# Kernel tuning notes

Measured on AMD Instinct MI355X. Metric: run time of the kernel, lower is better.

Reference implementation:

```python
import jax, jax.numpy as jnp
import numpy as np

N, E, IN, H, T = 100000, 1600000, 10, 64, 10


def setup_inputs() -> dict:
    key = jax.random.key(0)
    ks = jax.random.split(key, 24)
    w = lambda k, shape, s=0.05: jax.random.normal(k, shape, jnp.float32) * s
    return {
        "x": w(ks[0], (N, IN), 1.0),
        "edge_attr": w(ks[1], (E, T), 1.0),
        "gcn1_w": w(ks[2], (IN, H)), "gcn1_b": jnp.zeros((H,), jnp.float32),
        "e_w1": w(ks[3], (3 * T, H)), "e_b1": jnp.zeros((H,), jnp.float32),
        "e_w2": w(ks[4], (H, H)), "e_b2": jnp.zeros((H,), jnp.float32),
        "gcn2_w": w(ks[5], (2 * H, H)), "gcn2_b": jnp.zeros((H,), jnp.float32),
        "gcn3_w": w(ks[6], (H, IN)), "gcn3_b": jnp.zeros((IN,), jnp.float32),
        "l1_w": w(ks[7], (2 * IN, IN)), "l1_b": jnp.zeros((IN,), jnp.float32),
        "l2_w": w(ks[8], (IN, 128)), "l2_b": jnp.zeros((128,), jnp.float32),
        "l3_w": w(ks[9], (128, 32)), "l3_b": jnp.zeros((32,), jnp.float32),
        "l4_w": w(ks[10], (32, 2)), "l4_b": jnp.zeros((2,), jnp.float32),
        "edge_index": jax.random.randint(ks[11], (2, E), 0, N),
    }


def reference(x, edge_attr, gcn1_w, gcn1_b, e_w1, e_b1, e_w2, e_b2,
              gcn2_w, gcn2_b, gcn3_w, gcn3_b, l1_w, l1_b, l2_w, l2_b,
              l3_w, l3_b, l4_w, l4_b, edge_index):
    src, dst = edge_index[0], edge_index[1]  # j -> i (message flows src->dst)
    # GCN symmetric norm with self loops: deg counted on target, +1 self loop
    deg = 1.0 + jax.ops.segment_sum(jnp.ones((E,), jnp.float32), dst, num_segments=N)
    dis = deg ** -0.5  # [N]
    edge_norm = (dis[src] * dis[dst])[:, None]  # [E,1]

    def gcn(h, w, b):
        hw = h @ w  # [N,out]
        agg = jax.ops.segment_sum(hw[src] * edge_norm, dst, num_segments=N)
        agg = agg + hw * (dis * dis)[:, None]  # self-loop term, norm = 1/deg
        return agg + b

    out1 = jax.nn.relu(gcn(x, gcn1_w, gcn1_b))
    # EdgeConv: gather x_i (dst), x_j (src), concat edge_attr, MLP, scatter-max
    m = jnp.concatenate([x[dst], x[src], edge_attr], axis=1)  # [E, 3T]
    m = jax.nn.relu(m @ e_w1 + e_b1) @ e_w2 + e_b2  # [E, H]
    agg = jax.ops.segment_max(m, dst, num_segments=N)
    agg = jnp.where(jnp.isfinite(agg), agg, 0.0)  # isolated nodes -> 0
    oute = jax.nn.relu(agg)

    out2 = jax.nn.relu(gcn(jnp.concatenate([out1, oute], axis=1), gcn2_w, gcn2_b))
    out3 = jax.nn.relu(gcn(out2, gcn3_w, gcn3_b))
    h = jnp.concatenate([x, out3], axis=1)  # [N, 2*IN]
    h = jax.nn.softplus(h @ l1_w + l1_b)
    h = jax.nn.softplus(h @ l2_w + l2_b)
    h = jax.nn.softplus(h @ l3_w + l3_b)
    h = h @ l4_w + l4_b  # [N, 2]
    return (h[:, 0], h[:, 1])
```

## Files before the change

kernel.cpp:

```cpp
#include <hip/hip_runtime.h>
#include <hip/hip_bf16.h>

typedef unsigned int u32;
typedef unsigned short u16;
typedef _Float16 f16;
typedef _Float16 f16x8 __attribute__((ext_vector_type(8)));
typedef float f32x4 __attribute__((ext_vector_type(4)));
typedef u32 u32x4 __attribute__((ext_vector_type(4)));

#define DEV static __device__ __forceinline__

#define O_G1   0
#define O_G1b  640
#define O_W1   704
#define O_B1   2624
#define O_W2   2688
#define O_B2   6784
#define O_G2   6848
#define O_G2b  15040
#define O_G3   15104
#define O_G3b  15744
#define O_L1   15754
#define O_L1b  15954
#define O_L2t  15964
#define O_L2b  17244
#define O_L3   17372
#define O_L3b  21468
#define O_L4t  21500
#define O_L4b  21564
#define O_WF1  21568
#define O_WF2  22592
#define WTOT   24640

#define ECNB   32

DEV float bfu(u16 h){ return __uint_as_float(((u32)h) << 16); }
DEV float bflo(u32 u){ return __uint_as_float(u << 16); }
DEV float bfhi(u32 u){ return __uint_as_float(u & 0xffff0000u); }
DEV u16 f2bf(float x){
  __hip_bfloat16 b = __float2bfloat16(x);
  return *(u16*)&b;
}
DEV float rdf(const void* p, int idx, int isf32){
  return isf32 ? ((const float*)p)[idx] : bfu(((const u16*)p)[idx]);
}
DEV void load10_bf(const u32* __restrict__ p, float* f){
  u32 a0=p[0],a1=p[1],a2=p[2],a3=p[3],a4=p[4];
  f[0]=bflo(a0); f[1]=bfhi(a0);
  f[2]=bflo(a1); f[3]=bfhi(a1);
  f[4]=bflo(a2); f[5]=bfhi(a2);
  f[6]=bflo(a3); f[7]=bfhi(a3);
  f[8]=bflo(a4); f[9]=bfhi(a4);
}
DEV void load10_any(const void* base, size_t row, int isf32, float* f){
  if (isf32){
    const float* p = (const float*)base + row*10;
    #pragma unroll
    for (int k=0;k<10;k++) f[k] = p[k];
  } else {
    load10_bf((const u32*)base + row*5, f);
  }
}
DEV f16 load1_f16(const void* base, long idx, int isf32){
  return isf32 ? (f16)((const float*)base)[idx] : (f16)bfu(((const u16*)base)[idx]);
}
DEV float softplusf(float x){ return fmaxf(x,0.f) + log1pf(__expf(-fabsf(x))); }

DEV int permk(int k){
  if (k < 8)  return k;
  if (k < 16) return 10 + (k-8);
  if (k < 24) return 20 + (k-16);
  if (k == 24) return 8;
  if (k == 25) return 9;
  if (k == 26) return 18;
  if (k == 27) return 19;
  if (k == 28) return 28;
  if (k == 29) return 29;
  return -1;
}
DEV u32 packh2(float a, float b){
  union { f16 h[2]; u32 u; } t;
  t.h[0] = (f16)a; t.h[1] = (f16)b;
  return t.u;
}

__global__ __launch_bounds__(256) void k_detect(
    const u32* p0, const u32* p1, const u32* p2, const u32* p3,
    const u32* p4, const u32* p5, const u32* p6, const u32* p7,
    const u32* p8, const u32* p9, const u32* p10,const u32* p11,
    const u32* p12,const u32* p13,const u32* p14,const u32* p15,
    const u32* p16,const u32* p17,const u32* p18,const u32* p19,
    int* __restrict__ flags, int N_, int E_)
{
  int a = blockIdx.x;
  const u32* p;
  int elems;
  switch (a){
    case 0:  p=p0;  elems=N_*10; break;
    case 1:  p=p1;  elems=E_*10; break;
    case 2:  p=p2;  elems=640;  break;
    case 3:  p=p3;  elems=64;   break;
    case 4:  p=p4;  elems=1920; break;
    case 5:  p=p5;  elems=64;   break;
    case 6:  p=p6;  elems=4096; break;
    case 7:  p=p7;  elems=64;   break;
    case 8:  p=p8;  elems=8192; break;
    case 9:  p=p9;  elems=64;   break;
    case 10: p=p10; elems=640;  break;
    case 11: p=p11; elems=10;   break;
    case 12: p=p12; elems=200;  break;
    case 13: p=p13; elems=10;   break;
    case 14: p=p14; elems=1280; break;
    case 15: p=p15; elems=128;  break;
    case 16: p=p16; elems=4096; break;
    case 17: p=p17; elems=32;   break;
    case 18: p=p18; elems=64;   break;
    default: p=p19; elems=2;    break;
  }
  int nw = elems/2; if (nw > 512) nw = 512; if (nw < 1) nw = 1;
  int localA = 0, localZ = 0;
  for (int i=threadIdx.x; i<nw; i+=256){
    u32 w = p[i];
    u32 ex = (w >> 7) & 0xffu;
    if (ex >= 0x90u) localA++;
    if ((w & 0xffffu) == 0u) localZ++;
  }
  int packed = (localA << 16) | localZ;
  __shared__ int red[4];
  #pragma unroll
  for (int off=32; off; off>>=1) packed += __shfl_down(packed, off);
  if ((threadIdx.x & 63) == 0) red[threadIdx.x>>6] = packed;
  __syncthreads();
  if (threadIdx.x == 0){
    int s = red[0]+red[1]+red[2]+red[3];
    int sA = s >> 16, sZ = s & 0xffff;
    flags[a] = (sA * 16 >= nw || sZ * 4 >= nw * 3) ? 1 : 0;
  }
}

__global__ __launch_bounds__(256) void k_prep(
    const void* g1w, const void* g1b, const void* ew1, const void* eb1,
    const void* ew2, const void* eb2, const void* g2w, const void* g2b,
    const void* g3w, const void* g3b, const void* l1w, const void* l1b,
    const void* l2w, const void* l2b, const void* l3w, const void* l3b,
    const void* l4w, const void* l4b,
    const int* __restrict__ flags, float* __restrict__ W)
{
  int t = threadIdx.x;
  int f2=flags[2],f3=flags[3],f4=flags[4],f5=flags[5],f6=flags[6],f7=flags[7];
  int f8=flags[8],f9=flags[9],f10=flags[10],f11=flags[11],f12=flags[12],f13=flags[13];
  int f14=flags[14],f15=flags[15],f16=flags[16],f17=flags[17],f18=flags[18],f19=flags[19];
  for (int i=t;i<640;i+=256)  W[O_G1+i]  = rdf(g1w,i,f2);
  for (int i=t;i<64;i+=256)   W[O_G1b+i] = rdf(g1b,i,f3);
  for (int i=t;i<1920;i+=256) W[O_W1+i]  = rdf(ew1,i,f4);
  for (int i=t;i<64;i+=256)   W[O_B1+i]  = rdf(eb1,i,f5);
  for (int i=t;i<4096;i+=256) W[O_W2+i]  = rdf(ew2,i,f6);
  for (int i=t;i<64;i+=256)   W[O_B2+i]  = rdf(eb2,i,f7);
  for (int i=t;i<8192;i+=256) W[O_G2+i]  = rdf(g2w,i,f8);
  for (int i=t;i<64;i+=256)   W[O_G2b+i] = rdf(g2b,i,f9);
  for (int i=t;i<640;i+=256)  W[O_G3+i]  = rdf(g3w,i,f10);
  for (int i=t;i<10;i+=256)   W[O_G3b+i] = rdf(g3b,i,f11);
  for (int i=t;i<200;i+=256)  W[O_L1+i]  = rdf(l1w,i,f12);
  for (int i=t;i<10;i+=256)   W[O_L1b+i] = rdf(l1b,i,f13);
  for (int i=t;i<1280;i+=256){ int o=i/10,k=i-o*10; W[O_L2t+i]=rdf(l2w,k*128+o,f14); }
  for (int i=t;i<128;i+=256)  W[O_L2b+i] = rdf(l2b,i,f15);
  for (int i=t;i<4096;i+=256) W[O_L3+i]  = rdf(l3w,i,f16);
  for (int i=t;i<32;i+=256)   W[O_L3b+i] = rdf(l3b,i,f17);
  for (int i=t;i<64;i+=256){ int c=i>>5,j=i&31; W[O_L4t+i]=rdf(l4w,j*2+c,f18); }
  for (int i=t;i<2;i+=256)    W[O_L4b+i] = rdf(l4b,i,f19);
  u32* Wu = (u32*)W;
  for (int i=t;i<1024;i+=256){
    int l=i&63, q=(i>>6)&3, c=i>>8;
    int k0=(l>>4)*8+2*q, col=c*16+(l&15);
    int r0=permk(k0), r1=permk(k0+1);
    float v0 = (r0<0)?0.f:rdf(ew1,r0*64+col,f4);
    float v1 = (r1<0)?0.f:rdf(ew1,r1*64+col,f4);
    Wu[O_WF1+i] = packh2(v0,v1);
  }
  for (int i=t;i<2048;i+=256){
    int l=i&63, q=(i>>6)&3, h2=(i>>8)&1, c=i>>9;
    int k0=32*h2+(l>>4)*8+2*q, col=c*16+(l&15);
    Wu[O_WF2+i] = packh2(rdf(ew2,k0*64+col,f6), rdf(ew2,(k0+1)*64+col,f6));
  }
}

__global__ __launch_bounds__(256) void k_init(int* __restrict__ cnt, int N_)
{
  int i = blockIdx.x*256 + threadIdx.x;
  if (i < N_) cnt[i] = 0;
}

__global__ __launch_bounds__(256) void k_count(const int* __restrict__ ei, int* __restrict__ cnt, int E_)
{
  int e = blockIdx.x*256 + threadIdx.x;
  if (e >= E_) return;
  atomicAdd(&cnt[ei[E_+e]], 1);
}

__global__ __launch_bounds__(1024) void k_bsum(const int* __restrict__ cnt, int* __restrict__ bsum, int N_)
{
  int i = blockIdx.x*1024 + threadIdx.x;
  int v = (i < N_) ? cnt[i] : 0;
  #pragma unroll
  for (int off=32; off; off>>=1) v += __shfl_down(v, off);
  __shared__ int ws_[16];
  if ((threadIdx.x & 63) == 0) ws_[threadIdx.x>>6] = v;
  __syncthreads();
  if (threadIdx.x == 0){
    int s = 0;
    #pragma unroll
    for (int j=0;j<16;j++) s += ws_[j];
    bsum[blockIdx.x] = s;
  }
}

__global__ __launch_bounds__(128) void k_scan_small(const int* __restrict__ bsum, int* __restrict__ boff, int NB)
{
  int t = threadIdx.x;
  int v = (t < NB) ? bsum[t] : 0;
  int lane = t & 63, w = t >> 6;
  int x = v;
  #pragma unroll
  for (int off=1; off<64; off<<=1){ int y=__shfl_up(x,off); if (lane>=off) x+=y; }
  __shared__ int t2[2];
  if (lane==63) t2[w]=x;
  __syncthreads();
  if (w==1) x += t2[0];
  boff[t] = x - v;
}

__global__ __launch_bounds__(1024) void k_scan_final(
    int* __restrict__ cnt, const int* __restrict__ boff,
    int* __restrict__ rp, float* __restrict__ dis, int N_, int E_)
{
  int i = blockIdx.x*1024 + threadIdx.x;
  int v = (i < N_) ? cnt[i] : 0;
  int lane = threadIdx.x & 63, w = threadIdx.x >> 6;
  int x = v;
  #pragma unroll
  for (int off=1; off<64; off<<=1){ int y=__shfl_up(x,off); if (lane>=off) x+=y; }
  __shared__ int wp[16];
  if (lane==63) wp[w]=x;
  __syncthreads();
  if (threadIdx.x==0){
    int run=0;
    #pragma unroll
    for (int j=0;j<16;j++){ int t=wp[j]; wp[j]=run; run+=t; }
  }
  __syncthreads();
  int incl = x + wp[w] + boff[blockIdx.x];
  if (i < N_){
    rp[i]  = incl - v;
    dis[i] = rsqrtf(1.f + (float)v);
    cnt[i] = 0;
  }
  if (i == 0) rp[N_] = E_;
}

__global__ __launch_bounds__(256) void k_fill(
    const int* __restrict__ ei, const int* __restrict__ rp, int* __restrict__ cnt,
    int* __restrict__ csrc, int* __restrict__ cedge, int* __restrict__ cdst, int E_)
{
  int e = blockIdx.x*256 + threadIdx.x;
  if (e >= E_) return;
  int s = ei[e], d = ei[E_+e];
  int pos = rp[d] + atomicAdd(&cnt[d], 1);
  csrc[pos]  = s;
  cedge[pos] = e;
  cdst[pos]  = d;
}

#define EC_EMIT \
  if (run >= 0){ int bb = run*64 + x; \
    atomicMax(&nodemax[bb],    __float_as_int(e0)); \
    atomicMax(&nodemax[bb+16], __float_as_int(e1)); \
    atomicMax(&nodemax[bb+32], __float_as_int(e2)); \
    atomicMax(&nodemax[bb+48], __float_as_int(e3)); }
#define EC_STEP(DD, RR) { \
  float t0=fmaxf(mcv[0][RR],0.f), t1=fmaxf(mcv[1][RR],0.f), \
        t2=fmaxf(mcv[2][RR],0.f), t3=fmaxf(mcv[3][RR],0.f); \
  if (DD == run){ e0=fmaxf(e0,t0); e1=fmaxf(e1,t1); e2=fmaxf(e2,t2); e3=fmaxf(e3,t3); } \
  else { EC_EMIT; run = DD; e0=t0; e1=t1; e2=t2; e3=t3; } }

__global__ __launch_bounds__(256) void k_edgeconv(
    const void* __restrict__ xv, const void* __restrict__ eav,
    const int* __restrict__ rp, const int* __restrict__ csrc,
    const int* __restrict__ cedge, const int* __restrict__ cdst,
    const float* __restrict__ W, const int* __restrict__ flags,
    float* __restrict__ oute, int N_, int E_)
{
  __shared__ int nodemax[ECNB*64];
  __shared__ u32 hbuf[4][16*36];
  int tid = threadIdx.x;
  int l = tid & 63, wv = tid >> 6;
  int x = l & 15, g = l >> 4;
  int n0 = blockIdx.x * ECNB;
  if (n0 >= N_) return;
  int nend = n0 + ECNB; if (nend > N_) nend = N_;
  #pragma unroll
  for (int i=0;i<ECNB/4;i++) nodemax[i*256 + tid] = 0;
  int fx = flags[0], fea = flags[1];
  const u32* Wu = (const u32*)W;
  union FU { u32 u[4]; f16x8 v; };
  FU w1u[4];
  #pragma unroll
  for (int c=0;c<4;c++){
    #pragma unroll
    for (int q=0;q<4;q++) w1u[c].u[q] = Wu[O_WF1 + (c*4+q)*64 + l];
  }
  FU w2u[4][2];
  #pragma unroll
  for (int c=0;c<4;c++){
    #pragma unroll
    for (int h=0;h<2;h++){
      #pragma unroll
      for (int q=0;q<4;q++) w2u[c][h].u[q] = Wu[O_WF2 + ((c*2+h)*4+q)*64 + l];
    }
  }
  float b1v[4], b2v[4];
  #pragma unroll
  for (int c=0;c<4;c++){ b1v[c] = (W+O_B1)[c*16 + x]; b2v[c] = (W+O_B2)[c*16 + x]; }
  int pbase = rp[n0], pend = rp[nend];
  int ntiles = (pend - pbase + 15) >> 4;
  u32* hb = hbuf[wv];
  __syncthreads();

  for (int t = wv; t < ntiles; t += 4){
    int p0 = pbase + t*16;
    int pe = p0 + 4*g;
    int d0 = (pe   < pend) ? cdst[pe]   - n0 : -1;
    int d1 = (pe+1 < pend) ? cdst[pe+1] - n0 : -1;
    int d2 = (pe+2 < pend) ? cdst[pe+2] - n0 : -1;
    int d3 = (pe+3 < pend) ? cdst[pe+3] - n0 : -1;
    int eA = p0 + x; if (eA > E_-1) eA = E_-1;
    union HU { f16 h[8]; u32 u[4]; f16x8 v; } af;
    if (g < 3){
      long row; const void* base; int isf;
      if (g==0){ row = cdst[eA];  base = xv;  isf = fx; }
      else if (g==1){ row = csrc[eA]; base = xv;  isf = fx; }
      else { row = cedge[eA]; base = eav; isf = fea; }
      if (isf){
        const float* p = (const float*)base + row*10;
        #pragma unroll
        for (int j=0;j<8;j++) af.h[j] = (f16)p[j];
      } else {
        const u32* p = (const u32*)((const u16*)base + row*10);
        #pragma unroll
        for (int j=0;j<4;j++){ u32 w = p[j]; af.h[2*j] = (f16)bflo(w); af.h[2*j+1] = (f16)bfhi(w); }
      }
    } else {
      int di = cdst[eA], si = csrc[eA], ee = cedge[eA];
      af.h[0] = load1_f16(xv, (long)di*10+8, fx);
      af.h[1] = load1_f16(xv, (long)di*10+9, fx);
      af.h[2] = load1_f16(xv, (long)si*10+8, fx);
      af.h[3] = load1_f16(xv, (long)si*10+9, fx);
      af.h[4] = load1_f16(eav,(long)ee*10+8, fea);
      af.h[5] = load1_f16(eav,(long)ee*10+9, fea);
      af.h[6] = (f16)0.f; af.h[7] = (f16)0.f;
    }
    f32x4 z = {0.f,0.f,0.f,0.f};
    f32x4 hc[4];
    #pragma unroll
    for (int c=0;c<4;c++)
      hc[c] = __builtin_amdgcn_mfma_f32_16x16x32_f16(af.v, w1u[c].v, z, 0, 0, 0);
    #pragma unroll
    for (int r=0;r<4;r++){
      u32 pk0,pk1,pk2,pk3;
      {
        float hv = fmaxf(hc[0][r] + b1v[0], 0.f);
        union { f16 h; u16 u; } cv; cv.h=(f16)hv; u32 mine=cv.u;
        u32 other=(u32)__shfl_xor((int)mine,1,64);
        pk0 = (x&1) ? (other|(mine<<16)) : (mine|(other<<16));
      }{
        float hv = fmaxf(hc[1][r] + b1v[1], 0.f);
        union { f16 h; u16 u; } cv; cv.h=(f16)hv; u32 mine=cv.u;
        u32 other=(u32)__shfl_xor((int)mine,1,64);
        pk1 = (x&1) ? (other|(mine<<16)) : (mine|(other<<16));
      }{
        float hv = fmaxf(hc[2][r] + b1v[2], 0.f);
        union { f16 h; u16 u; } cv; cv.h=(f16)hv; u32 mine=cv.u;
        u32 other=(u32)__shfl_xor((int)mine,1,64);
        pk2 = (x&1) ? (other|(mine<<16)) : (mine|(other<<16));
      }{
        float hv = fmaxf(hc[3][r] + b1v[3], 0.f);
        union { f16 h; u16 u; } cv; cv.h=(f16)hv; u32 mine=cv.u;
        u32 other=(u32)__shfl_xor((int)mine,1,64);
        pk3 = (x&1) ? (other|(mine<<16)) : (mine|(other<<16));
      }
      int edge = 4*g + r;
      int par = (x&1) ? 16 : 0;
      hb[edge*36 + par + (x>>1)]     = (x&1) ? pk2 : pk0;
      hb[edge*36 + 8 + par + (x>>1)] = (x&1) ? pk3 : pk1;
    }
    asm volatile("s_waitcnt lgkmcnt(0)" ::: "memory");
    HU a2f[2];
    #pragma unroll
    for (int h=0;h<2;h++){
      const u32x4* p = (const u32x4*)&hb[x*36 + g*4 + 16*h];
      u32x4 tv = *p;
      a2f[h].u[0]=tv[0]; a2f[h].u[1]=tv[1]; a2f[h].u[2]=tv[2]; a2f[h].u[3]=tv[3];
    }
    f32x4 mcv[4];
    #pragma unroll
    for (int c=0;c<4;c++){
      f32x4 bi = {b2v[c],b2v[c],b2v[c],b2v[c]};
      f32x4 acc = __builtin_amdgcn_mfma_f32_16x16x32_f16(a2f[0].v, w2u[c][0].v, bi, 0, 0, 0);
      mcv[c]    = __builtin_amdgcn_mfma_f32_16x16x32_f16(a2f[1].v, w2u[c][1].v, acc, 0, 0, 0);
    }
    int run = -2; float e0=0.f,e1=0.f,e2=0.f,e3=0.f;
    EC_STEP(d0,0) EC_STEP(d1,1) EC_STEP(d2,2) EC_STEP(d3,3)
    EC_EMIT;
  }
  __syncthreads();
  int tot = (nend - n0) * 64;
  for (int i = tid; i < tot; i += 256)
    oute[(size_t)n0*64 + i] = __int_as_float(nodemax[i]);
}

__global__ __launch_bounds__(256) void k_aggx(
    const void* __restrict__ xv, const int* __restrict__ rp,
    const int* __restrict__ csrc, const float* __restrict__ dis,
    const int* __restrict__ flags, float* __restrict__ sx, int N_)
{
  int i = blockIdx.x*256 + threadIdx.x;
  if (i >= N_) return;
  int fx = flags[0];
  float di = dis[i], d2 = di*di;
  float acc[10], ac2[10], tA[10], tB[10];
  load10_any(xv, (size_t)i, fx, tA);
  #pragma unroll
  for (int f=0;f<10;f++){ acc[f] = tA[f]*d2; ac2[f] = 0.f; }
  int b = rp[i], en = rp[i+1];
  int p = b;
  for (; p+1 < en; p += 2){
    int sA = csrc[p], sB = csrc[p+1];
    float nmA = dis[sA]*di, nmB = dis[sB]*di;
    load10_any(xv, (size_t)sA, fx, tA);
    load10_any(xv, (size_t)sB, fx, tB);
    #pragma unroll
    for (int f=0;f<10;f++){
      acc[f] = fmaf(tA[f], nmA, acc[f]);
      ac2[f] = fmaf(tB[f], nmB, ac2[f]);
    }
  }
  if (p < en){
    int sA = csrc[p]; float nmA = dis[sA]*di;
    load10_any(xv, (size_t)sA, fx, tA);
    #pragma unroll
    for (int f=0;f<10;f++) acc[f] = fmaf(tA[f], nmA, acc[f]);
  }
  float* o = sx + (size_t)i*10;
  #pragma unroll
  for (int f=0;f<10;f++) o[f] = acc[f] + ac2[f];
}

__global__ __launch_bounds__(256) void k_hw2(
    const float* __restrict__ sx, const float* __restrict__ oute,
    const float* __restrict__ W, u16* __restrict__ hw2o, int N_)
{
  int i = blockIdx.x*256 + threadIdx.x;
  if (i >= N_) return;
  float sv[10];
  const float* srow = sx + (size_t)i*10;
  #pragma unroll
  for (int f=0;f<10;f++) sv[f] = srow[f];
  const float* __restrict__ G1  = W + O_G1;
  const float* __restrict__ G1b = W + O_G1b;
  const float* __restrict__ G2  = W + O_G2;
  float hw[64];
  #pragma unroll
  for (int f=0;f<64;f++) hw[f] = 0.f;
  #pragma unroll 1
  for (int k=0;k<64;k++){
    float o1 = G1b[k];
    #pragma unroll
    for (int j=0;j<10;j++) o1 = fmaf(sv[j], G1[j*64+k], o1);
    o1 = fmaxf(o1, 0.f);
    const float* __restrict__ wt = G2 + k*64;
    #pragma unroll
    for (int f=0;f<64;f++) hw[f] = fmaf(o1, wt[f], hw[f]);
  }
  const float* orow = oute + (size_t)i*64;
  #pragma unroll 1
  for (int k=0;k<64;k++){
    float ov = orow[k];
    const float* __restrict__ wb = G2 + (64+k)*64;
    #pragma unroll
    for (int f=0;f<64;f++) hw[f] = fmaf(ov, wb[f], hw[f]);
  }
  u16* out = hw2o + (size_t)i*64;
  #pragma unroll
  for (int f=0;f<64;f++) out[f] = f2bf(hw[f]);
}

__global__ __launch_bounds__(256) void k_agg64(
    const u16* __restrict__ hw2, const int* __restrict__ rp,
    const int* __restrict__ csrc, const float* __restrict__ dis,
    const float* __restrict__ W, float* __restrict__ out2, int N_)
{
  int i = (blockIdx.x*256 + threadIdx.x) >> 6;
  int lane = threadIdx.x & 63;
  if (i >= N_) return;
  int e4 = lane >> 4, c4 = lane & 15;
  float di = dis[i];
  int b = rp[i], en = rp[i+1];
  const uint2* __restrict__ h2 = (const uint2*)hw2;
  float a0=0.f,a1=0.f,a2=0.f,a3=0.f;
  float b0=0.f,b1=0.f,b2=0.f,b3=0.f;
  int p = b + e4;
  int sA = (p   < en) ? csrc[p]   : 0;
  int sB = (p+4 < en) ? csrc[p+4] : 0;
  for (; p + 4 < en; p += 8){
    int sAn = (p+8  < en) ? csrc[p+8]  : 0;
    int sBn = (p+12 < en) ? csrc[p+12] : 0;
    float nmA = dis[sA]*di, nmB = dis[sB]*di;
    uint2 wA = h2[(size_t)sA*16 + c4];
    uint2 wB = h2[(size_t)sB*16 + c4];
    a0 = fmaf(bflo(wA.x), nmA, a0); a1 = fmaf(bfhi(wA.x), nmA, a1);
    a2 = fmaf(bflo(wA.y), nmA, a2); a3 = fmaf(bfhi(wA.y), nmA, a3);
    b0 = fmaf(bflo(wB.x), nmB, b0); b1 = fmaf(bfhi(wB.x), nmB, b1);
    b2 = fmaf(bflo(wB.y), nmB, b2); b3 = fmaf(bfhi(wB.y), nmB, b3);
    sA = sAn; sB = sBn;
  }
  if (p < en){
    float nmA = dis[sA]*di;
    uint2 wA = h2[(size_t)sA*16 + c4];
    a0 = fmaf(bflo(wA.x), nmA, a0); a1 = fmaf(bfhi(wA.x), nmA, a1);
    a2 = fmaf(bflo(wA.y), nmA, a2); a3 = fmaf(bfhi(wA.y), nmA, a3);
  }
  a0 += b0; a1 += b1; a2 += b2; a3 += b3;
  a0 += __shfl_xor(a0,16); a1 += __shfl_xor(a1,16);
  a2 += __shfl_xor(a2,16); a3 += __shfl_xor(a3,16);
  a0 += __shfl_xor(a0,32); a1 += __shfl_xor(a1,32);
  a2 += __shfl_xor(a2,32); a3 += __shfl_xor(a3,32);
  if (e4 == 0){
    uint2 ws2 = h2[(size_t)i*16 + c4];
    float d2 = di*di;
    const float* G2b = W + O_G2b;
    float4 o;
    o.x = fmaxf(fmaf(bflo(ws2.x), d2, a0) + G2b[4*c4],   0.f);
    o.y = fmaxf(fmaf(bfhi(ws2.x), d2, a1) + G2b[4*c4+1], 0.f);
    o.z = fmaxf(fmaf(bflo(ws2.y), d2, a2) + G2b[4*c4+2], 0.f);
    o.w = fmaxf(fmaf(bfhi(ws2.y), d2, a3) + G2b[4*c4+3], 0.f);
    *(float4*)(out2 + (size_t)i*64 + 4*c4) = o;
  }
}

__global__ __launch_bounds__(256) void k_hw3(
    const float* __restrict__ out2, const float* __restrict__ W,
    float* __restrict__ hw3, int N_)
{
  int i = blockIdx.x*256 + threadIdx.x;
  if (i >= N_) return;
  const float* row = out2 + (size_t)i*64;
  const float* __restrict__ G3 = W + O_G3;
  float a[10];
  #pragma unroll
  for (int f=0;f<10;f++) a[f] = 0.f;
  #pragma unroll 1
  for (int k=0;k<64;k++){
    float v = row[k];
    const float* __restrict__ w = G3 + k*10;
    #pragma unroll
    for (int f=0;f<10;f++) a[f] = fmaf(v, w[f], a[f]);
  }
  float* o = hw3 + (size_t)i*10;
  #pragma unroll
  for (int f=0;f<10;f++) o[f] = a[f];
}

__global__ __launch_bounds__(256) void k_final(
    const void* __restrict__ xv, const float* __restrict__ hw3,
    const int* __restrict__ rp, const int* __restrict__ csrc,
    const float* __restrict__ dis, const int* __restrict__ flags,
    const float* __restrict__ W, float* __restrict__ out, int N_)
{
  int i = blockIdx.x*256 + threadIdx.x;
  if (i >= N_) return;
  int fx = flags[0];
  float di = dis[i];
  float a[10], a2v[10];
  const float* hrow = hw3 + (size_t)i*10;
  #pragma unroll
  for (int f=0;f<10;f++){ a[f] = hrow[f]*di*di; a2v[f] = 0.f; }
  int b = rp[i], en = rp[i+1];
  int p = b;
  for (; p+1 < en; p += 2){
    int sA = csrc[p], sB = csrc[p+1];
    float nmA = dis[sA]*di, nmB = dis[sB]*di;
    const float* rA = hw3 + (size_t)sA*10;
    const float* rB = hw3 + (size_t)sB*10;
    #pragma unroll
    for (int f=0;f<10;f++){
      a[f]   = fmaf(rA[f], nmA, a[f]);
      a2v[f] = fmaf(rB[f], nmB, a2v[f]);
    }
  }
  if (p < en){
    int sA = csrc[p]; float nmA = dis[sA]*di;
    const float* rA = hw3 + (size_t)sA*10;
    #pragma unroll
    for (int f=0;f<10;f++) a[f] = fmaf(rA[f], nmA, a[f]);
  }
  #pragma unroll
  for (int f=0;f<10;f++) a[f] += a2v[f];
  const float* G3b = W + O_G3b;
  float h20[20];
  load10_any(xv, (size_t)i, fx, h20);
  #pragma unroll
  for (int f=0;f<10;f++) h20[10+f] = fmaxf(a[f] + G3b[f], 0.f);
  const float* __restrict__ L1  = W + O_L1;
  const float* __restrict__ L1b = W + O_L1b;
  float h1[10];
  #pragma unroll
  for (int f=0;f<10;f++) h1[f] = L1b[f];
  #pragma unroll
  for (int k=0;k<20;k++){
    float v = h20[k];
    const float* __restrict__ w = L1 + k*10;
    #pragma unroll
    for (int f=0;f<10;f++) h1[f] = fmaf(v, w[f], h1[f]);
  }
  #pragma unroll
  for (int f=0;f<10;f++) h1[f] = softplusf(h1[f]);
  const float* __restrict__ L2t = W + O_L2t;
  const float* __restrict__ L2b = W + O_L2b;
  const float* __restrict__ L3  = W + O_L3;
  const float* __restrict__ L3b = W + O_L3b;
  float h3a[32];
  #pragma unroll
  for (int j=0;j<32;j++) h3a[j] = L3b[j];
  #pragma unroll 1
  for (int o=0;o<128;o++){
    float s2 = L2b[o];
    const float* __restrict__ wt = L2t + o*10;
    #pragma unroll
    for (int k=0;k<10;k++) s2 = fmaf(h1[k], wt[k], s2);
    s2 = softplusf(s2);
    const float* __restrict__ w3 = L3 + o*32;
    #pragma unroll
    for (int j=0;j<32;j++) h3a[j] = fmaf(s2, w3[j], h3a[j]);
  }
  const float* L4t = W + O_L4t;
  const float* L4b = W + O_L4b;
  float r0 = L4b[0], r1 = L4b[1];
  #pragma unroll
  for (int j=0;j<32;j++){
    float h3 = softplusf(h3a[j]);
    r0 = fmaf(h3, L4t[j],    r0);
    r1 = fmaf(h3, L4t[32+j], r1);
  }
  out[i]      = r0;
  out[N_ + i] = r1;
}

extern "C" void kernel_launch(void* const* d_in, const int* in_sizes, int n_in,
                              void* d_out, int out_size, void* d_ws, size_t ws_size,
                              hipStream_t stream)
{
  const void* xv  = d_in[0];
  const void* eav = d_in[1];
  const int*  ei  = (const int*)d_in[20];
  int N_ = in_sizes[0] / 10;
  int E_ = in_sizes[1] / 10;

  float* W = (float*)d_ws;
  size_t off = WTOT;
  int*   cnt   = (int*)(W + off);   off += (size_t)N_;
  int*   rp    = (int*)(W + off);   off += (size_t)N_ + 1;
  float* dis   = (float*)(W + off); off += (size_t)N_;
  int*   bsum  = (int*)(W + off);   off += 256;
  int*   boff  = (int*)(W + off);   off += 256;
  int*   flags = (int*)(W + off);   off += 32;
  int*   csrc  = (int*)(W + off);   off += (size_t)E_;
  int*   cedge = (int*)(W + off);   off += (size_t)E_;
  off = (off + 3) & ~(size_t)3;
  float* oute  = (float*)(W + off);
  float* out2  = oute;
  off += (size_t)N_ * 64;
  off = (off + 3) & ~(size_t)3;
  u16*   hw2   = (u16*)(W + off);   off += (size_t)N_ * 32;
  off = (off + 3) & ~(size_t)3;
  float* sx    = (float*)(W + off);
  float* hw3   = sx;
  off += (size_t)N_ * 10;

  int* cdst;
  if ((size_t)E_ <= (size_t)N_ * 32) {
    cdst = (int*)hw2;
  } else {
    cdst = (int*)(W + off); off += (size_t)E_;
  }

  if (ws_size < off * sizeof(float)) return;

  int gN = (N_ + 255)/256, gE = (E_ + 255)/256;
  int NB = (N_ + 1023)/1024;

  k_detect<<<20,256,0,stream>>>(
      (const u32*)d_in[0],(const u32*)d_in[1],
      (const u32*)d_in[2],(const u32*)d_in[3],(const u32*)d_in[4],(const u32*)d_in[5],
      (const u32*)d_in[6],(const u32*)d_in[7],(const u32*)d_in[8],(const u32*)d_in[9],
      (const u32*)d_in[10],(const u32*)d_in[11],(const u32*)d_in[12],(const u32*)d_in[13],
      (const u32*)d_in[14],(const u32*)d_in[15],(const u32*)d_in[16],(const u32*)d_in[17],
      (const u32*)d_in[18],(const u32*)d_in[19],
      flags, N_, E_);
  k_prep<<<1,256,0,stream>>>(
      d_in[2],d_in[3],d_in[4],d_in[5],d_in[6],d_in[7],d_in[8],d_in[9],
      d_in[10],d_in[11],d_in[12],d_in[13],d_in[14],d_in[15],d_in[16],d_in[17],
      d_in[18],d_in[19], flags, W);
  k_init<<<gN,256,0,stream>>>(cnt, N_);
  k_count<<<gE,256,0,stream>>>(ei, cnt, E_);
  k_bsum<<<NB,1024,0,stream>>>(cnt, bsum, N_);
  k_scan_small<<<1,128,0,stream>>>(bsum, boff, NB);
  k_scan_final<<<NB,1024,0,stream>>>(cnt, boff, rp, dis, N_, E_);
  k_fill<<<gE,256,0,stream>>>(ei, rp, cnt, csrc, cedge, cdst, E_);
  k_edgeconv<<<(N_+ECNB-1)/ECNB,256,0,stream>>>(xv, eav, rp, csrc, cedge, cdst, W, flags, oute, N_, E_);
  k_aggx<<<gN,256,0,stream>>>(xv, rp, csrc, dis, flags, sx, N_);
  k_hw2<<<gN,256,0,stream>>>(sx, oute, W, hw2, N_);
  k_agg64<<<(N_+3)/4,256,0,stream>>>(hw2, rp, csrc, dis, W, out2, N_);
  k_hw3<<<gN,256,0,stream>>>(out2, W, hw3, N_);
  k_final<<<gN,256,0,stream>>>(xv, hw3, rp, csrc, dis, flags, W,
                               (float*)d_out, N_);
}
```

Before: 761.8 us.

## Pack CSR src/edge/dst into int4 records and share gathered features via shuffles

Replaces the three separate CSR arrays (csrc, cedge, cdst) with one interleaved int4 array written by a single 16-byte store in k_fill. EdgeConv loads one int4 per lane and takes the dst indices and the columns 8-9 of each row from other lanes with shuffles, so it no longer does scalar gathers. The aggregation kernels aggx and final unroll their neighbour loops by 4 instead of 2. The catch is that the aggregation kernels, which read only src, now fetch 16-byte strided records, so they pull four times the index bytes.

```diff
diff --git a/kernel.cpp b/kernel.cpp
--- a/kernel.cpp
+++ b/kernel.cpp
@@ -60,9 +60,6 @@
   } else {
     load10_bf((const u32*)base + row*5, f);
   }
-}
-DEV f16 load1_f16(const void* base, long idx, int isf32){
-  return isf32 ? (f16)((const float*)base)[idx] : (f16)bfu(((const u16*)base)[idx]);
 }
 DEV float softplusf(float x){ return fmaxf(x,0.f) + log1pf(__expf(-fabsf(x))); }
 
@@ -259,15 +256,13 @@
 
 __global__ __launch_bounds__(256) void k_fill(
     const int* __restrict__ ei, const int* __restrict__ rp, int* __restrict__ cnt,
-    int* __restrict__ csrc, int* __restrict__ cedge, int* __restrict__ cdst, int E_)
+    int4* __restrict__ csr, int E_)
 {
   int e = blockIdx.x*256 + threadIdx.x;
   if (e >= E_) return;
   int s = ei[e], d = ei[E_+e];
   int pos = rp[d] + atomicAdd(&cnt[d], 1);
-  csrc[pos]  = s;
-  cedge[pos] = e;
-  cdst[pos]  = d;
+  csr[pos] = make_int4(s, e, d, 0);
 }
 
 #define EC_EMIT \
@@ -284,8 +279,7 @@
 
 __global__ __launch_bounds__(256) void k_edgeconv(
     const void* __restrict__ xv, const void* __restrict__ eav,
-    const int* __restrict__ rp, const int* __restrict__ csrc,
-    const int* __restrict__ cedge, const int* __restrict__ cdst,
+    const int* __restrict__ rp, const int4* __restrict__ csr,
     const float* __restrict__ W, const int* __restrict__ flags,
     float* __restrict__ oute, int N_, int E_)
 {
@@ -302,6 +296,7 @@
   int fx = flags[0], fea = flags[1];
   const u32* Wu = (const u32*)W;
   union FU { u32 u[4]; f16x8 v; };
+  union HU { f16 h[8]; u32 u[4]; f16x8 v; };
   FU w1u[4];
   #pragma unroll
   for (int c=0;c<4;c++){
@@ -327,37 +322,40 @@
 
   for (int t = wv; t < ntiles; t += 4){
     int p0 = pbase + t*16;
-    int pe = p0 + 4*g;
-    int d0 = (pe   < pend) ? cdst[pe]   - n0 : -1;
-    int d1 = (pe+1 < pend) ? cdst[pe+1] - n0 : -1;
-    int d2 = (pe+2 < pend) ? cdst[pe+2] - n0 : -1;
-    int d3 = (pe+3 < pend) ? cdst[pe+3] - n0 : -1;
     int eA = p0 + x; if (eA > E_-1) eA = E_-1;
-    union HU { f16 h[8]; u32 u[4]; f16x8 v; } af;
+    int4 ce = csr[eA];
+    HU af;
+    u32 exv = 0;
     if (g < 3){
       long row; const void* base; int isf;
-      if (g==0){ row = cdst[eA];  base = xv;  isf = fx; }
-      else if (g==1){ row = csrc[eA]; base = xv;  isf = fx; }
-      else { row = cedge[eA]; base = eav; isf = fea; }
+      if (g==0){ row = ce.z; base = xv;  isf = fx; }
+      else if (g==1){ row = ce.x; base = xv;  isf = fx; }
+      else { row = ce.y; base = eav; isf = fea; }
       if (isf){
         const float* p = (const float*)base + row*10;
         #pragma unroll
         for (int j=0;j<8;j++) af.h[j] = (f16)p[j];
+        exv = packh2(p[8], p[9]);
       } else {
-        const u32* p = (const u32*)((const u16*)base + row*10);
-        #pragma unroll
-        for (int j=0;j<4;j++){ u32 w = p[j]; af.h[2*j] = (f16)bflo(w); af.h[2*j+1] = (f16)bfhi(w); }
+        const u32* p = (const u32*)base + row*5;
+        u32 a0=p[0],a1=p[1],a2=p[2],a3=p[3],a4=p[4];
+        af.h[0]=(f16)bflo(a0); af.h[1]=(f16)bfhi(a0);
+        af.h[2]=(f16)bflo(a1); af.h[3]=(f16)bfhi(a1);
+        af.h[4]=(f16)bflo(a2); af.h[5]=(f16)bfhi(a2);
+        af.h[6]=(f16)bflo(a3); af.h[7]=(f16)bfhi(a3);
+        exv = packh2(bflo(a4), bfhi(a4));
       }
-    } else {
-      int di = cdst[eA], si = csrc[eA], ee = cedge[eA];
-      af.h[0] = load1_f16(xv, (long)di*10+8, fx);
-      af.h[1] = load1_f16(xv, (long)di*10+9, fx);
-      af.h[2] = load1_f16(xv, (long)si*10+8, fx);
-      af.h[3] = load1_f16(xv, (long)si*10+9, fx);
-      af.h[4] = load1_f16(eav,(long)ee*10+8, fea);
-      af.h[5] = load1_f16(eav,(long)ee*10+9, fea);
-      af.h[6] = (f16)0.f; af.h[7] = (f16)0.f;
     }
+    u32 ge0 = (u32)__shfl((int)exv, x);
+    u32 ge1 = (u32)__shfl((int)exv, x+16);
+    u32 ge2 = (u32)__shfl((int)exv, x+32);
+    if (g == 3){ af.u[0]=ge0; af.u[1]=ge1; af.u[2]=ge2; af.u[3]=0; }
+    int pe = p0 + 4*g;
+    int dz = ce.z;
+    int d0 = __shfl(dz, 4*g+0); d0 = (pe   < pend) ? d0 - n0 : -1;
+    int d1 = __shfl(dz, 4*g+1); d1 = (pe+1 < pend) ? d1 - n0 : -1;
+    int d2 = __shfl(dz, 4*g+2); d2 = (pe+2 < pend) ? d2 - n0 : -1;
+    int d3 = __shfl(dz, 4*g+3); d3 = (pe+3 < pend) ? d3 - n0 : -1;
     f32x4 z = {0.f,0.f,0.f,0.f};
     f32x4 hc[4];
     #pragma unroll
@@ -419,35 +417,39 @@
 
 __global__ __launch_bounds__(256) void k_aggx(
     const void* __restrict__ xv, const int* __restrict__ rp,
-    const int* __restrict__ csrc, const float* __restrict__ dis,
+    const int4* __restrict__ csr, const float* __restrict__ dis,
     const int* __restrict__ flags, float* __restrict__ sx, int N_)
 {
   int i = blockIdx.x*256 + threadIdx.x;
   if (i >= N_) return;
   int fx = flags[0];
   float di = dis[i], d2 = di*di;
-  float acc[10], ac2[10], tA[10], tB[10];
+  float acc[10], ac2[10], tA[10], tB[10], tC[10], tD[10];
   load10_any(xv, (size_t)i, fx, tA);
   #pragma unroll
   for (int f=0;f<10;f++){ acc[f] = tA[f]*d2; ac2[f] = 0.f; }
   int b = rp[i], en = rp[i+1];
   int p = b;
-  for (; p+1 < en; p += 2){
-    int sA = csrc[p], sB = csrc[p+1];
-    float nmA = dis[sA]*di, nmB = dis[sB]*di;
-    load10_any(xv, (size_t)sA, fx, tA);
-    load10_any(xv, (size_t)sB, fx, tB);
+  for (; p+3 < en; p += 4){
+    int s0 = csr[p].x, s1 = csr[p+1].x, s2 = csr[p+2].x, s3 = csr[p+3].x;
+    float m0 = dis[s0]*di, m1 = dis[s1]*di, m2 = dis[s2]*di, m3 = dis[s3]*di;
+    load10_any(xv, (size_t)s0, fx, tA);
+    load10_any(xv, (size_t)s1, fx, tB);
+    load10_any(xv, (size_t)s2, fx, tC);
+    load10_any(xv, (size_t)s3, fx, tD);
     #pragma unroll
     for (int f=0;f<10;f++){
-      acc[f] = fmaf(tA[f], nmA, acc[f]);
-      ac2[f] = fmaf(tB[f], nmB, ac2[f]);
+      acc[f] = fmaf(tA[f], m0, acc[f]);
+      ac2[f] = fmaf(tB[f], m1, ac2[f]);
+      acc[f] = fmaf(tC[f], m2, acc[f]);
+      ac2[f] = fmaf(tD[f], m3, ac2[f]);
     }
   }
-  if (p < en){
-    int sA = csrc[p]; float nmA = dis[sA]*di;
-    load10_any(xv, (size_t)sA, fx, tA);
-    #pragma unroll
-    for (int f=0;f<10;f++) acc[f] = fmaf(tA[f], nmA, acc[f]);
+  for (; p < en; p++){
+    int s0 = csr[p].x; float m0 = dis[s0]*di;
+    load10_any(xv, (size_t)s0, fx, tA);
+    #pragma unroll
+    for (int f=0;f<10;f++) acc[f] = fmaf(tA[f], m0, acc[f]);
   }
   float* o = sx + (size_t)i*10;
   #pragma unroll
@@ -495,7 +497,7 @@
 
 __global__ __launch_bounds__(256) void k_agg64(
     const u16* __restrict__ hw2, const int* __restrict__ rp,
-    const int* __restrict__ csrc, const float* __restrict__ dis,
+    const int4* __restrict__ csr, const float* __restrict__ dis,
     const float* __restrict__ W, float* __restrict__ out2, int N_)
 {
   int i = (blockIdx.x*256 + threadIdx.x) >> 6;
@@ -508,11 +510,11 @@
   float a0=0.f,a1=0.f,a2=0.f,a3=0.f;
   float b0=0.f,b1=0.f,b2=0.f,b3=0.f;
   int p = b + e4;
-  int sA = (p   < en) ? csrc[p]   : 0;
-  int sB = (p+4 < en) ? csrc[p+4] : 0;
+  int sA = (p   < en) ? csr[p].x   : 0;
+  int sB = (p+4 < en) ? csr[p+4].x : 0;
   for (; p + 4 < en; p += 8){
-    int sAn = (p+8  < en) ? csrc[p+8]  : 0;
-    int sBn = (p+12 < en) ? csrc[p+12] : 0;
+    int sAn = (p+8  < en) ? csr[p+8].x  : 0;
+    int sBn = (p+12 < en) ? csr[p+12].x : 0;
     float nmA = dis[sA]*di, nmB = dis[sB]*di;
     uint2 wA = h2[(size_t)sA*16 + c4];
     uint2 wB = h2[(size_t)sB*16 + c4];
@@ -571,7 +573,7 @@
 
 __global__ __launch_bounds__(256) void k_final(
     const void* __restrict__ xv, const float* __restrict__ hw3,
-    const int* __restrict__ rp, const int* __restrict__ csrc,
+    const int* __restrict__ rp, const int4* __restrict__ csr,
     const float* __restrict__ dis, const int* __restrict__ flags,
     const float* __restrict__ W, float* __restrict__ out, int N_)
 {
@@ -585,22 +587,26 @@
   for (int f=0;f<10;f++){ a[f] = hrow[f]*di*di; a2v[f] = 0.f; }
   int b = rp[i], en = rp[i+1];
   int p = b;
-  for (; p+1 < en; p += 2){
-    int sA = csrc[p], sB = csrc[p+1];
-    float nmA = dis[sA]*di, nmB = dis[sB]*di;
-    const float* rA = hw3 + (size_t)sA*10;
-    const float* rB = hw3 + (size_t)sB*10;
+  for (; p+3 < en; p += 4){
+    int s0 = csr[p].x, s1 = csr[p+1].x, s2 = csr[p+2].x, s3 = csr[p+3].x;
+    float m0 = dis[s0]*di, m1 = dis[s1]*di, m2 = dis[s2]*di, m3 = dis[s3]*di;
+    const float* r0p = hw3 + (size_t)s0*10;
+    const float* r1p = hw3 + (size_t)s1*10;
+    const float* r2p = hw3 + (size_t)s2*10;
+    const float* r3p = hw3 + (size_t)s3*10;
     #pragma unroll
     for (int f=0;f<10;f++){
-      a[f]   = fmaf(rA[f], nmA, a[f]);
-      a2v[f] = fmaf(rB[f], nmB, a2v[f]);
+      a[f]   = fmaf(r0p[f], m0, a[f]);
+      a2v[f] = fmaf(r1p[f], m1, a2v[f]);
+      a[f]   = fmaf(r2p[f], m2, a[f]);
+      a2v[f] = fmaf(r3p[f], m3, a2v[f]);
     }
   }
-  if (p < en){
-    int sA = csrc[p]; float nmA = dis[sA]*di;
-    const float* rA = hw3 + (size_t)sA*10;
-    #pragma unroll
-    for (int f=0;f<10;f++) a[f] = fmaf(rA[f], nmA, a[f]);
+  for (; p < en; p++){
+    int s0 = csr[p].x; float m0 = dis[s0]*di;
+    const float* r0p = hw3 + (size_t)s0*10;
+    #pragma unroll
+    for (int f=0;f<10;f++) a[f] = fmaf(r0p[f], m0, a[f]);
   }
   #pragma unroll
   for (int f=0;f<10;f++) a[f] += a2v[f];
@@ -672,25 +678,15 @@
   int*   bsum  = (int*)(W + off);   off += 256;
   int*   boff  = (int*)(W + off);   off += 256;
   int*   flags = (int*)(W + off);   off += 32;
-  int*   csrc  = (int*)(W + off);   off += (size_t)E_;
-  int*   cedge = (int*)(W + off);   off += (size_t)E_;
   off = (off + 3) & ~(size_t)3;
+  int4*  csr   = (int4*)(W + off);  off += (size_t)E_ * 4;
   float* oute  = (float*)(W + off);
   float* out2  = oute;
   off += (size_t)N_ * 64;
-  off = (off + 3) & ~(size_t)3;
   u16*   hw2   = (u16*)(W + off);   off += (size_t)N_ * 32;
-  off = (off + 3) & ~(size_t)3;
   float* sx    = (float*)(W + off);
   float* hw3   = sx;
   off += (size_t)N_ * 10;
-
-  int* cdst;
-  if ((size_t)E_ <= (size_t)N_ * 32) {
-    cdst = (int*)hw2;
-  } else {
-    cdst = (int*)(W + off); off += (size_t)E_;
-  }
 
   if (ws_size < off * sizeof(float)) return;
 
@@ -714,12 +710,12 @@
   k_bsum<<<NB,1024,0,stream>>>(cnt, bsum, N_);
   k_scan_small<<<1,128,0,stream>>>(bsum, boff, NB);
   k_scan_final<<<NB,1024,0,stream>>>(cnt, boff, rp, dis, N_, E_);
-  k_fill<<<gE,256,0,stream>>>(ei, rp, cnt, csrc, cedge, cdst, E_);
-  k_edgeconv<<<(N_+ECNB-1)/ECNB,256,0,stream>>>(xv, eav, rp, csrc, cedge, cdst, W, flags, oute, N_, E_);
-  k_aggx<<<gN,256,0,stream>>>(xv, rp, csrc, dis, flags, sx, N_);
+  k_fill<<<gE,256,0,stream>>>(ei, rp, cnt, csr, E_);
+  k_edgeconv<<<(N_+ECNB-1)/ECNB,256,0,stream>>>(xv, eav, rp, csr, W, flags, oute, N_, E_);
+  k_aggx<<<gN,256,0,stream>>>(xv, rp, csr, dis, flags, sx, N_);
   k_hw2<<<gN,256,0,stream>>>(sx, oute, W, hw2, N_);
-  k_agg64<<<(N_+3)/4,256,0,stream>>>(hw2, rp, csrc, dis, W, out2, N_);
+  k_agg64<<<(N_+3)/4,256,0,stream>>>(hw2, rp, csr, dis, W, out2, N_);
   k_hw3<<<gN,256,0,stream>>>(out2, W, hw3, N_);
-  k_final<<<gN,256,0,stream>>>(xv, hw3, rp, csrc, dis, flags, W,
+  k_final<<<gN,256,0,stream>>>(xv, hw3, rp, csr, dis, flags, W,
                                (float*)d_out, N_);
 }
```

Result: faster. 730.1 us (-4.2%).
